# Kernel tuning notes

Hardware: AMD Instinct MI355X
Metric: run time of the kernel (lower is better)

Reference implementation:

```python
import math
import jax, jax.numpy as jnp
import numpy as np

HIDDEN = 768
HEADS = 12
HEAD_DIM = HIDDEN // HEADS  # 64
NUM_BUCKETS = 32            # T5-style relative position bias defaults
MAX_DIST = 128
EPS = 1e-6


def _rel_buckets(T):
    # T5 bidirectional relative-position bucketing, computed statically in numpy.
    ctx = np.arange(T)[:, None]
    mem = np.arange(T)[None, :]
    rp = mem - ctx                     # (T, T)
    nb = NUM_BUCKETS // 2
    ret = (rp > 0).astype(np.int64) * nb
    n = np.abs(rp)
    max_exact = nb // 2
    is_small = n < max_exact
    val_large = max_exact + (
        np.log(np.maximum(n, 1) / max_exact) / math.log(MAX_DIST / max_exact) * (nb - max_exact)
    ).astype(np.int64)
    val_large = np.minimum(val_large, nb - 1)
    ret = ret + np.where(is_small, n, val_large)
    return ret  # (T, T) int


def _layernorm(x, scale, bias):
    mu = jnp.mean(x, axis=-1, keepdims=True)
    var = jnp.mean((x - mu) ** 2, axis=-1, keepdims=True)
    return (x - mu) * jax.lax.rsqrt(var + EPS) * scale + bias


def _rms_groupnorm(x, weight):
    # x: (N, C, H, W, D); RMS over (channels-in-group, spatial), per-channel scale.
    N, C, H, W, D = x.shape
    xg = x.reshape(N, HEADS, C // HEADS, H, W, D)
    ms = jnp.mean(xg * xg, axis=(2, 3, 4, 5), keepdims=True)
    xg = xg * jax.lax.rsqrt(ms + EPS)
    return xg.reshape(N, C, H, W, D) * weight[None, :, None, None, None]


def _forward(x, norm1_weight, input_head_weight, input_head_bias,
             qnorm_scale, qnorm_bias, knorm_scale, knorm_bias,
             rel_bias_table, output_head_weight, output_head_bias):
    T, B, C, H, W, D = x.shape
    residual = x
    xn = _rms_groupnorm(x.reshape(T * B, C, H, W, D), norm1_weight)
    # 1x1 conv QKV as channels-last matmul
    w_in = input_head_weight[:, :, 0, 0, 0]                       # (3C, C)
    xt = jnp.transpose(xn, (0, 2, 3, 4, 1))                        # (TB, H, W, D, C)
    qkv = xt @ w_in.T + input_head_bias                            # (TB, H, W, D, 3C)
    # '(t b) (he c) h w d -> (b h w d) he t c'  with c = 3*head_dim
    qkv = qkv.reshape(T, B, H, W, D, HEADS, 3 * HEAD_DIM)
    qkv = jnp.transpose(qkv, (1, 2, 3, 4, 5, 0, 6))                # (B,H,W,D,He,T,3hd)
    qkv = qkv.reshape(B * H * W * D, HEADS, T, 3 * HEAD_DIM)
    q, k, v = jnp.split(qkv, 3, axis=-1)                           # each (N, He, T, hd)
    q = _layernorm(q, qnorm_scale, qnorm_bias)
    k = _layernorm(k, knorm_scale, knorm_bias)
    # relative position bias (bidirectional)
    buckets = jnp.asarray(_rel_buckets(T))                         # (T, T)
    bias = jnp.transpose(rel_bias_table[buckets], (2, 0, 1))[None]  # (1, He, T, T)
    scale = 1.0 / math.sqrt(HEAD_DIM)
    attn = jax.nn.softmax(jnp.einsum('bhsc,bhtc->bhst', q, k) * scale + bias, axis=-1)
    out = jnp.einsum('bhst,bhtc->bhsc', attn, v)                   # (N, He, T, hd)
    # '(b h w d) he t c -> (t b) (he c) h w d'
    out = out.reshape(B, H, W, D, HEADS, T, HEAD_DIM)
    out = jnp.transpose(out, (5, 0, 4, 6, 1, 2, 3))                # (T,B,He,hd,H,W,D)
    out = out.reshape(T * B, C, H, W, D)
    # output 1x1 conv
    w_out = output_head_weight[:, :, 0, 0, 0]                      # (C, C)
    ot = jnp.transpose(out, (0, 2, 3, 4, 1)) @ w_out.T + output_head_bias
    y = jnp.transpose(ot, (0, 4, 1, 2, 3)).reshape(T, B, C, H, W, D)
    return y + residual


def setup_inputs() -> dict:
    key = jax.random.key(0)
    ks = jax.random.split(key, 4)
    T, B, C, H, W, D = 16, 1, HIDDEN, 16, 16, 8
    x = jax.random.normal(ks[0], (T, B, C, H, W, D), dtype=jnp.float32)
    lecun = 1.0 / math.sqrt(HIDDEN)
    return {
        'x': x,
        'norm1_weight': jnp.ones((HIDDEN,), jnp.float32),
        'input_head_weight': jax.random.normal(ks[1], (3 * HIDDEN, HIDDEN, 1, 1, 1), jnp.float32) * lecun,
        'input_head_bias': jnp.zeros((3 * HIDDEN,), jnp.float32),
        'qnorm_scale': jnp.ones((HEAD_DIM,), jnp.float32),
        'qnorm_bias': jnp.zeros((HEAD_DIM,), jnp.float32),
        'knorm_scale': jnp.ones((HEAD_DIM,), jnp.float32),
        'knorm_bias': jnp.zeros((HEAD_DIM,), jnp.float32),
        'rel_bias_table': jax.random.normal(ks[2], (NUM_BUCKETS, HEADS), jnp.float32) * 0.02,
        'output_head_weight': jax.random.normal(ks[3], (HIDDEN, HIDDEN, 1, 1, 1), jnp.float32) * lecun,
        'output_head_bias': jnp.zeros((HIDDEN,), jnp.float32),
    }


def reference(x, norm1_weight, input_head_weight, input_head_bias,
              qnorm_scale, qnorm_bias, knorm_scale, knorm_bias,
              rel_bias_table, output_head_weight, output_head_bias):
    return _forward(x, norm1_weight, input_head_weight, input_head_bias,
                    qnorm_scale, qnorm_bias, knorm_scale, knorm_bias,
                    rel_bias_table, output_head_weight, output_head_bias)
```

## Files before the change

### kernel.cpp

```cpp
#include <hip/hip_runtime.h>
#include <stdint.h>

#define Tt 16
#define Cc 768
#define Ss 2048
#define N1 2304
#define NH 12
#define HD 64
#define EPSV 1e-6f

typedef unsigned short ushort_t;
typedef __attribute__((ext_vector_type(8))) short short8;
typedef __attribute__((ext_vector_type(4))) short short4v;
typedef __attribute__((ext_vector_type(4))) float f32x4;

static __device__ __forceinline__ float b2f(unsigned short u) {
  union { unsigned int i; float f; } c;
  c.i = ((unsigned int)u) << 16;
  return c.f;
}
static __device__ __forceinline__ unsigned short f2b(float f) {
  union { float f; unsigned int i; } c;
  c.f = f;
  return (unsigned short)((c.i + 0x7fffu + ((c.i >> 16) & 1u)) >> 16);
}

static __device__ __forceinline__ void load8(const void* p, size_t eoff,
                                             int isf32, float* o) {
  if (isf32) {
    const float* f = (const float*)p + eoff;
    f32x4 a = *(const f32x4*)f;
    f32x4 b = *(const f32x4*)(f + 4);
    o[0] = a[0]; o[1] = a[1]; o[2] = a[2]; o[3] = a[3];
    o[4] = b[0]; o[5] = b[1]; o[6] = b[2]; o[7] = b[3];
  } else {
    short8 d = *(const short8*)((const ushort_t*)p + eoff);
#pragma unroll
    for (int e = 0; e < 8; e++) o[e] = b2f((unsigned short)d[e]);
  }
}
static __device__ __forceinline__ float load1(const void* p, size_t eoff, int isf32) {
  return isf32 ? ((const float*)p)[eoff] : b2f(((const ushort_t*)p)[eoff]);
}

#define GLP(p) ((const __attribute__((address_space(1))) void*)(p))
#define LDSP(p) ((__attribute__((address_space(3))) void*)(p))

__global__ __launch_bounds__(256) void detect_k(const ushort_t* __restrict__ x,
                                               int* __restrict__ flag) {
  __shared__ int sbad;
  if (threadIdx.x == 0) sbad = 0;
  __syncthreads();
  int bad = 0;
  for (int i = threadIdx.x; i < 65536; i += 256) {
    const unsigned int e = (x[i] >> 7) & 0xFFu;
    if (e == 0xFFu) bad = 1;
  }
  if (bad) atomicOr(&sbad, 1);
  __syncthreads();
  if (threadIdx.x == 0) flag[0] = sbad;
}

__global__ __launch_bounds__(256) void cvt_big_k(const void* __restrict__ src,
                                                ushort_t* __restrict__ dst,
                                                int n8, const int* __restrict__ flag) {
  const int isf32 = *flag;
  const int i = blockIdx.x * 256 + threadIdx.x;
  if (i >= n8) return;
  float o[8];
  load8(src, (size_t)i * 8, isf32, o);
  short8 v;
#pragma unroll
  for (int e = 0; e < 8; e++) v[e] = (short)f2b(o[e]);
  *(short8*)(dst + (size_t)i * 8) = v;
}

__global__ __launch_bounds__(256) void cvt_small_k(
    const void* w1, const void* bin, const void* bo, const void* qs,
    const void* qb, const void* ks, const void* kb, const void* relb,
    ushort_t* __restrict__ dst, const int* __restrict__ flag) {
  const int isf32 = *flag;
  const void* srcs[8] = {w1, bin, bo, qs, qb, ks, kb, relb};
  const int sizes[8] = {768, 2304, 768, 64, 64, 64, 64, 384};
  int off = 0;
#pragma unroll
  for (int s = 0; s < 8; s++) {
    for (int i = threadIdx.x; i < sizes[s]; i += 256)
      dst[off + i] = isf32 ? f2b(((const float*)srcs[s])[i])
                           : ((const ushort_t*)srcs[s])[i];
    off += sizes[s];
  }
}

__global__ __launch_bounds__(256) void rms_stats_k(
    const void* __restrict__ x, const int* __restrict__ flag,
    float* __restrict__ invrms) {
  const int isf32 = *flag;
  const int t = blockIdx.x / NH;
  const int g = blockIdx.x % NH;
  const size_t base = ((size_t)(t * Cc + g * 64)) * Ss;
  float ss = 0.f;
  for (int v = threadIdx.x; v < 16384; v += 256) {
    const int ci = v >> 8;
    const int sj = (v & 255) << 3;
    float o[8];
    load8(x, base + (size_t)ci * Ss + sj, isf32, o);
#pragma unroll
    for (int e = 0; e < 8; e++) ss += o[e] * o[e];
  }
#pragma unroll
  for (int m = 1; m < 64; m <<= 1) ss += __shfl_xor(ss, m);
  __shared__ float red[4];
  if ((threadIdx.x & 63) == 0) red[threadIdx.x >> 6] = ss;
  __syncthreads();
  if (threadIdx.x == 0) {
    float tot = red[0] + red[1] + red[2] + red[3];
    invrms[blockIdx.x] = rsqrtf(tot * (1.f / 131072.f) + EPSV);
  }
}

__global__ __launch_bounds__(256) void norm_chunk_k(
    const void* __restrict__ x, const int* __restrict__ flag,
    const ushort_t* __restrict__ w1, const float* __restrict__ invrms,
    ushort_t* __restrict__ xnc, int s0c, int chl) {
  __shared__ __align__(16) ushort_t tile[64][64];
  const int isf32 = *flag;
  const int t = blockIdx.z;
  const int c0 = blockIdx.y * 64;
  const int sl0 = blockIdx.x * 64;
  const float ir = invrms[t * NH + (c0 >> 6)];
  const int tid = threadIdx.x;
  for (int v = tid; v < 512; v += 256) {
    const int ci = v >> 3;
    const int q = v & 7;
    float o[8];
    load8(x, ((size_t)(t * Cc + c0 + ci)) * Ss + s0c + sl0 + q * 8, isf32, o);
    const float sc = ir * b2f(w1[c0 + ci]);
    short8 w;
#pragma unroll
    for (int e = 0; e < 8; e++) w[e] = (short)f2b(o[e] * sc);
    *(short8*)&tile[ci][(q ^ (ci >> 3)) * 8] = w;
  }
  __syncthreads();
  for (int v = tid; v < 512; v += 256) {
    const int sj = v >> 3;
    const int cb = (v & 7) * 8;
    const int sw = (sj >> 3) ^ (v & 7);
    const int so = sj & 7;
    short8 o;
#pragma unroll
    for (int e = 0; e < 8; e++) o[e] = (short)tile[cb + e][sw * 8 + so];
    *(short8*)(xnc + ((size_t)(t * chl + sl0 + sj)) * Cc + c0 + cb) = o;
  }
}

__global__ __launch_bounds__(256, 2) void gemm_qkv_k(
    const ushort_t* __restrict__ A, const ushort_t* __restrict__ Bw,
    const ushort_t* __restrict__ bias, ushort_t* __restrict__ Cout) {
  __shared__ __align__(16) ushort_t As[128 * 32];
  __shared__ __align__(16) ushort_t Bs[128 * 32];
  const int tid = threadIdx.x;
  const int bm0 = blockIdx.x * 128;
  const int bn0 = blockIdx.y * 128;
  const int lane = tid & 63;
  const int wave = tid >> 6;
  const int wm = (wave >> 1) << 6;
  const int wn = (wave & 1) << 6;
  f32x4 acc[4][4];
#pragma unroll
  for (int i = 0; i < 4; i++)
#pragma unroll
    for (int j = 0; j < 4; j++) acc[i][j] = (f32x4){0.f, 0.f, 0.f, 0.f};
  const int srow = tid >> 2;
  const int scol = (tid & 3) << 3;
  const ushort_t* ag = A + (size_t)(bm0 + srow) * Cc + scol;
  const ushort_t* bg = Bw + (size_t)(bn0 + srow) * Cc + scol;
  ushort_t* la = As + tid * 8;
  ushort_t* lb = Bs + tid * 8;
  const int frow = lane & 15;
  const int koff = (lane >> 4) << 3;
  for (int kt = 0; kt < Cc; kt += 32) {
    __syncthreads();
    __builtin_amdgcn_global_load_lds(GLP(ag + kt), LDSP(la), 16, 0, 0);
    __builtin_amdgcn_global_load_lds(GLP(ag + kt + 64 * Cc), LDSP(la + 2048), 16, 0, 0);
    __builtin_amdgcn_global_load_lds(GLP(bg + kt), LDSP(lb), 16, 0, 0);
    __builtin_amdgcn_global_load_lds(GLP(bg + kt + 64 * Cc), LDSP(lb + 2048), 16, 0, 0);
    __syncthreads();
    short8 af[4], bf[4];
#pragma unroll
    for (int i = 0; i < 4; i++)
      af[i] = *(const short8*)(As + (wm + i * 16 + frow) * 32 + koff);
#pragma unroll
    for (int j = 0; j < 4; j++)
      bf[j] = *(const short8*)(Bs + (wn + j * 16 + frow) * 32 + koff);
#pragma unroll
    for (int i = 0; i < 4; i++)
#pragma unroll
      for (int j = 0; j < 4; j++)
        acc[i][j] = __builtin_amdgcn_mfma_f32_16x16x32_bf16(af[i], bf[j], acc[i][j], 0, 0, 0);
  }
  const int mq = (lane >> 4) << 2;
  const int nl = lane & 15;
#pragma unroll
  for (int j = 0; j < 4; j++) {
    const int col = bn0 + wn + j * 16 + nl;
    const float bc = b2f(bias[col]);
#pragma unroll
    for (int i = 0; i < 4; i++) {
#pragma unroll
      for (int r = 0; r < 4; r++) {
        const int row = bm0 + wm + i * 16 + mq + r;
        Cout[(size_t)row * N1 + col] = f2b(acc[i][j][r] + bc);
      }
    }
  }
}

static __device__ __forceinline__ void rdA_q(short8 af[4][2], const ushort_t* base,
                                             int arow, int half, const int ckk[2]) {
#pragma unroll
  for (int mi = 0; mi < 4; mi++)
#pragma unroll
    for (int kk = 0; kk < 2; kk++)
      af[mi][kk] = *(const short8*)&base[arow + half * 4096 + mi * 1024 + ckk[kk]];
}
static __device__ __forceinline__ void rdB_q(short8 bf[2][2], const ushort_t* base,
                                             int brow, int nib, const int ckk[2]) {
#pragma unroll
  for (int ni = 0; ni < 2; ni++)
#pragma unroll
    for (int kk = 0; kk < 2; kk++)
      bf[ni][kk] = *(const short8*)&base[brow + (nib + ni) * 1024 + ckk[kk]];
}
template <int MIB, int NIB>
static __device__ __forceinline__ void mm8_q(f32x4 (&acc)[8][4], const short8 af[4][2],
                                             const short8 bf[2][2]) {
#pragma unroll
  for (int mi = 0; mi < 4; mi++)
#pragma unroll
    for (int ni = 0; ni < 2; ni++)
#pragma unroll
      for (int kk = 0; kk < 2; kk++)
        acc[MIB + mi][NIB + ni] = __builtin_amdgcn_mfma_f32_16x16x32_bf16(
            af[mi][kk], bf[ni][kk], acc[MIB + mi][NIB + ni], 0, 0, 0);
}

__global__ __launch_bounds__(512, 2) void gemm_qkv256_k(
    const ushort_t* __restrict__ A, const ushort_t* __restrict__ Bw,
    const ushort_t* __restrict__ bias, ushort_t* __restrict__ Cout) {
  __shared__ __align__(16) ushort_t lds[2][2][16384];
  const int tid = threadIdx.x;
  const int lane = tid & 63;
  const int wave = tid >> 6;
  const int wr = wave >> 2;
  const int wc = wave & 3;
  const int wg = ((int)blockIdx.x & 7) * 144 + ((int)blockIdx.x >> 3);
  const int bm0 = (wg / 9) * 256;
  const int bn0 = (wg % 9) * 256;
  const int srow = tid >> 3;
  const int scol = ((tid & 7) ^ (srow & 7)) << 3;
  const ushort_t* ag = A + (size_t)(bm0 + srow) * Cc + scol;
  const ushort_t* bg = Bw + (size_t)(bn0 + srow) * Cc + scol;
#define QSTG(p, kt) { \
    __builtin_amdgcn_global_load_lds(GLP(ag + (kt)), LDSP(&lds[p][0][tid * 8]), 16, 0, 0); \
    __builtin_amdgcn_global_load_lds(GLP(ag + 64 * Cc + (kt)), LDSP(&lds[p][0][4096 + tid * 8]), 16, 0, 0); \
    __builtin_amdgcn_global_load_lds(GLP(ag + 128 * Cc + (kt)), LDSP(&lds[p][0][8192 + tid * 8]), 16, 0, 0); \
    __builtin_amdgcn_global_load_lds(GLP(ag + 192 * Cc + (kt)), LDSP(&lds[p][0][12288 + tid * 8]), 16, 0, 0); \
    __builtin_amdgcn_global_load_lds(GLP(bg + (kt)), LDSP(&lds[p][1][tid * 8]), 16, 0, 0); \
    __builtin_amdgcn_global_load_lds(GLP(bg + 64 * Cc + (kt)), LDSP(&lds[p][1][4096 + tid * 8]), 16, 0, 0); \
    __builtin_amdgcn_global_load_lds(GLP(bg + 128 * Cc + (kt)), LDSP(&lds[p][1][8192 + tid * 8]), 16, 0, 0); \
    __builtin_amdgcn_global_load_lds(GLP(bg + 192 * Cc + (kt)), LDSP(&lds[p][1][12288 + tid * 8]), 16, 0, 0); \
  }
  const int koffb = (lane >> 4) << 4;
  const int lsw = (lane & 7) << 4;
  const int ckk[2] = {(koffb ^ lsw) >> 1, ((64 + koffb) ^ lsw) >> 1};
  const int arow = (wr * 128 + (lane & 15)) * 64;
  const int brow = (wc * 64 + (lane & 15)) * 64;
  f32x4 acc[8][4];
#pragma unroll
  for (int i = 0; i < 8; i++)
#pragma unroll
    for (int j = 0; j < 4; j++) acc[i][j] = (f32x4){0.f, 0.f, 0.f, 0.f};
  QSTG(0, 0);
  __syncthreads();
  for (int i = 0; i < 12; i++) {
    const int p = i & 1;
    if (i < 11) QSTG(p ^ 1, (i + 1) * 64);
    __builtin_amdgcn_sched_barrier(0);
    const ushort_t* Ab = &lds[p][0][0];
    const ushort_t* Bb = &lds[p][1][0];
    short8 af[4][2], bf0[2][2], bf1[2][2];
    rdA_q(af, Ab, arow, 0, ckk);
    rdB_q(bf0, Bb, brow, 0, ckk);
    __builtin_amdgcn_s_setprio(1);
    mm8_q<0, 0>(acc, af, bf0);
    __builtin_amdgcn_s_setprio(0);
    __builtin_amdgcn_sched_barrier(0);
    rdB_q(bf1, Bb, brow, 2, ckk);
    __builtin_amdgcn_s_setprio(1);
    mm8_q<0, 2>(acc, af, bf1);
    __builtin_amdgcn_s_setprio(0);
    __builtin_amdgcn_sched_barrier(0);
    rdA_q(af, Ab, arow, 1, ckk);
    __builtin_amdgcn_s_setprio(1);
    mm8_q<4, 0>(acc, af, bf0);
    __builtin_amdgcn_s_setprio(0);
    __builtin_amdgcn_sched_barrier(0);
    __builtin_amdgcn_s_setprio(1);
    mm8_q<4, 2>(acc, af, bf1);
    __builtin_amdgcn_s_setprio(0);
    if (i < 11) __syncthreads();
  }
  const int mq = (lane >> 4) << 2;
  const int nl = lane & 15;
#pragma unroll
  for (int ni = 0; ni < 4; ni++) {
    const int col = bn0 + wc * 64 + ni * 16 + nl;
    const float bc = b2f(bias[col]);
#pragma unroll
    for (int mi = 0; mi < 8; mi++) {
#pragma unroll
      for (int r = 0; r < 4; r++) {
        const int row = bm0 + wr * 128 + mi * 16 + mq + r;
        Cout[(size_t)row * N1 + col] = f2b(acc[mi][ni][r] + bc);
      }
    }
  }
#undef QSTG
}

__global__ __launch_bounds__(256) void attention_k(
    const ushort_t* __restrict__ qkvc, const ushort_t* __restrict__ qs,
    const ushort_t* __restrict__ qb, const ushort_t* __restrict__ ks,
    const ushort_t* __restrict__ kb, const ushort_t* __restrict__ relb,
    ushort_t* __restrict__ aoc, int chl) {
  __shared__ __align__(16) float qf[4][16][68];
  __shared__ __align__(16) float kf[4][16][68];
  __shared__ __align__(16) float vf[4][16][68];
  __shared__ __align__(16) float attw[4][16][20];
  __shared__ __align__(16) float lnw[4][64];
  const int tid = threadIdx.x;
  const int wave = tid >> 6;
  const int lane = tid & 63;
  if (tid < 64) {
    lnw[0][tid] = b2f(qs[tid]);
    lnw[1][tid] = b2f(qb[tid]);
    lnw[2][tid] = b2f(ks[tid]);
    lnw[3][tid] = b2f(kb[tid]);
  }
  const int p = blockIdx.x * 4 + wave;
  const int sl = p / 12;
  const int h = p - sl * 12;
  const ushort_t* src = qkvc + (size_t)sl * N1 + h * 192;
  const size_t tstride = (size_t)chl * N1;
#pragma unroll
  for (int t = 0; t < 16; t++) {
    const ushort_t* r = src + (size_t)t * tstride;
    qf[wave][t][lane] = b2f(r[lane]);
    kf[wave][t][lane] = b2f(r[64 + lane]);
    vf[wave][t][lane] = b2f(r[128 + lane]);
  }
  __syncthreads();
  {
    const int row = lane >> 1;
    const int half = lane & 1;
    float* buf = (row < 16) ? &qf[wave][row][0] : &kf[wave][row - 16][0];
    const float* sc = (row < 16) ? lnw[0] : lnw[2];
    const float* bi = (row < 16) ? lnw[1] : lnw[3];
    f32x4* bp = (f32x4*)(buf + half * 32);
    f32x4 v4[8];
    float s = 0.f;
#pragma unroll
    for (int q4 = 0; q4 < 8; q4++) {
      v4[q4] = bp[q4];
      s += v4[q4][0] + v4[q4][1] + v4[q4][2] + v4[q4][3];
    }
    s += __shfl_xor(s, 1);
    const float mu = s * (1.f / 64.f);
    float va = 0.f;
#pragma unroll
    for (int q4 = 0; q4 < 8; q4++) {
#pragma unroll
      for (int e = 0; e < 4; e++) {
        const float d = v4[q4][e] - mu;
        va += d * d;
      }
    }
    va += __shfl_xor(va, 1);
    const float rs = rsqrtf(va * (1.f / 64.f) + EPSV);
    const f32x4* sc4 = (const f32x4*)(sc + half * 32);
    const f32x4* bi4 = (const f32x4*)(bi + half * 32);
#pragma unroll
    for (int q4 = 0; q4 < 8; q4++) {
      f32x4 scv = sc4[q4], biv = bi4[q4], o;
#pragma unroll
      for (int e = 0; e < 4; e++) o[e] = (v4[q4][e] - mu) * rs * scv[e] + biv[e];
      bp[q4] = o;
    }
  }
  __syncthreads();
  const int g = lane >> 4;
  const int t2 = lane & 15;
#pragma unroll
  for (int it = 0; it < 4; it++) {
    const int t1 = it * 4 + g;
    const f32x4* qrow = (const f32x4*)&qf[wave][t1][0];
    const f32x4* krow = (const f32x4*)&kf[wave][t2][0];
    float sco = 0.f;
#pragma unroll
    for (int q4 = 0; q4 < 16; q4++) {
      f32x4 a = qrow[q4], b = krow[q4];
      sco += a[0] * b[0] + a[1] * b[1] + a[2] * b[2] + a[3] * b[3];
    }
    const int rp = t2 - t1;
    int bkt = (rp > 0) ? 16 : 0;
    const int n = (rp < 0) ? -rp : rp;
    if (n < 8) {
      bkt += n;
    } else {
      int vl = 8 + (int)(__logf((float)n * 0.125f) * 2.8853900817779268f);
      bkt += (vl < 15) ? vl : 15;
    }
    sco = sco * 0.125f + b2f(relb[bkt * NH + h]);
    float mx = sco;
#pragma unroll
    for (int m = 8; m >= 1; m >>= 1) mx = fmaxf(mx, __shfl_xor(mx, m));
    const float ex = __expf(sco - mx);
    float sm = ex;
#pragma unroll
    for (int m = 8; m >= 1; m >>= 1) sm += __shfl_xor(sm, m);
    attw[wave][t1][t2] = ex / sm;
  }
  __syncthreads();
  const int jq = lane & 15;
#pragma unroll
  for (int it = 0; it < 4; it++) {
    const int t1 = it * 4 + g;
    const f32x4* arow2 = (const f32x4*)&attw[wave][t1][0];
    f32x4 o = (f32x4){0.f, 0.f, 0.f, 0.f};
#pragma unroll
    for (int tq = 0; tq < 4; tq++) {
      f32x4 aw = arow2[tq];
#pragma unroll
      for (int e = 0; e < 4; e++) {
        f32x4 vv = *(const f32x4*)&vf[wave][tq * 4 + e][jq * 4];
        o[0] += aw[e] * vv[0];
        o[1] += aw[e] * vv[1];
        o[2] += aw[e] * vv[2];
        o[3] += aw[e] * vv[3];
      }
    }
    short4v st;
#pragma unroll
    for (int e = 0; e < 4; e++) st[e] = (short)f2b(o[e]);
    *(short4v*)(aoc + ((size_t)(t1 * chl + sl)) * Cc + h * HD + jq * 4) = st;
  }
}

__global__ __launch_bounds__(256, 2) void gemm_out_k(
    const ushort_t* __restrict__ A, const ushort_t* __restrict__ Bm,
    const ushort_t* __restrict__ bias, const void* __restrict__ xres,
    const int* __restrict__ flag, float* __restrict__ y, int s0c,
    int chl, int lgchl) {
  __shared__ __align__(16) ushort_t As[128 * 32];
  __shared__ __align__(16) ushort_t Bs[128 * 32];
  const int isf32 = *flag;
  const int tid = threadIdx.x;
  int bmt = blockIdx.x, bnt = blockIdx.y;
  {
    const int nwg = gridDim.x * gridDim.y;
    if ((nwg & 7) == 0) {
      const int hw = (int)blockIdx.x + (int)blockIdx.y * gridDim.x;
      const int cpx = nwg >> 3;
      const int w = (hw & 7) * cpx + (hw >> 3);
      bmt = w % gridDim.x;
      bnt = w / gridDim.x;
    }
  }
  const int bm0 = bmt * 128;
  const int bn0 = bnt * 128;
  const int lane = tid & 63;
  const int wave = tid >> 6;
  const int wm = (wave >> 1) << 6;
  const int wn = (wave & 1) << 6;
  f32x4 acc[4][4];
#pragma unroll
  for (int i = 0; i < 4; i++)
#pragma unroll
    for (int j = 0; j < 4; j++) acc[i][j] = (f32x4){0.f, 0.f, 0.f, 0.f};
  const int srow = tid >> 2;
  const int scol = (tid & 3) << 3;
  const ushort_t* ag = A + (size_t)(bm0 + srow) * Cc + scol;
  const ushort_t* bg = Bm + (size_t)(bn0 + srow) * Cc + scol;
  ushort_t* la = As + tid * 8;
  ushort_t* lb = Bs + tid * 8;
  const int frow = lane & 15;
  const int koff = (lane >> 4) << 3;
  for (int kt = 0; kt < Cc; kt += 32) {
    __syncthreads();
    __builtin_amdgcn_global_load_lds(GLP(ag + kt), LDSP(la), 16, 0, 0);
    __builtin_amdgcn_global_load_lds(GLP(ag + kt + 64 * Cc), LDSP(la + 2048), 16, 0, 0);
    __builtin_amdgcn_global_load_lds(GLP(bg + kt), LDSP(lb), 16, 0, 0);
    __builtin_amdgcn_global_load_lds(GLP(bg + kt + 64 * Cc), LDSP(lb + 2048), 16, 0, 0);
    __syncthreads();
    short8 af[4], bf[4];
#pragma unroll
    for (int i = 0; i < 4; i++)
      af[i] = *(const short8*)(As + (wm + i * 16 + frow) * 32 + koff);
#pragma unroll
    for (int j = 0; j < 4; j++)
      bf[j] = *(const short8*)(Bs + (wn + j * 16 + frow) * 32 + koff);
#pragma unroll
    for (int i = 0; i < 4; i++)
#pragma unroll
      for (int j = 0; j < 4; j++)
        acc[i][j] = __builtin_amdgcn_mfma_f32_16x16x32_bf16(af[i], bf[j], acc[i][j], 0, 0, 0);
  }
  const int mq = (lane >> 4) << 2;
  const int nl = lane & 15;
#pragma unroll
  for (int j = 0; j < 4; j++) {
    const int col = bn0 + wn + j * 16 + nl;
    const int t = col >> lgchl;
    const int sp = s0c + (col & (chl - 1));
#pragma unroll
    for (int i = 0; i < 4; i++) {
#pragma unroll
      for (int r = 0; r < 4; r++) {
        const int cch = bm0 + wm + i * 16 + mq + r;
        const size_t off = ((size_t)(t * Cc + cch)) * Ss + sp;
        y[off] = acc[i][j][r] + b2f(bias[cch]) + load1(xres, off, isf32);
      }
    }
  }
}

extern "C" void kernel_launch(void* const* d_in, const int* in_sizes, int n_in,
                              void* d_out, int out_size, void* d_ws, size_t ws_size,
                              hipStream_t stream) {
  (void)in_sizes; (void)n_in; (void)out_size;
  const void* x   = d_in[0];
  const void* w1  = d_in[1];
  const void* win = d_in[2];
  const void* bin = d_in[3];
  const void* qsc = d_in[4];
  const void* qbi = d_in[5];
  const void* ksc = d_in[6];
  const void* kbi = d_in[7];
  const void* rbt = d_in[8];
  const void* wo  = d_in[9];
  const void* bo  = d_in[10];
  float* y = (float*)d_out;

  char* ws = (char*)d_ws;
  int* flag      = (int*)ws;
  ushort_t* smallw = (ushort_t*)(ws + 4096);
  ushort_t* w1b  = smallw;
  ushort_t* binb = smallw + 768;
  ushort_t* bob  = smallw + 3072;
  ushort_t* qsb  = smallw + 3840;
  ushort_t* qbb  = smallw + 3904;
  ushort_t* ksb  = smallw + 3968;
  ushort_t* kbb  = smallw + 4032;
  ushort_t* relbb = smallw + 4096;
  float* invrms  = (float*)(ws + 1024);
  ushort_t* winb = (ushort_t*)(ws + 20480);
  ushort_t* wob  = (ushort_t*)(ws + 3559424);
  const size_t fixed = 4739072;

  const size_t per_row = (size_t)(Cc * 2 + N1 * 2 + Cc * 2);
  int chl = Ss;
  while (chl > 64 && fixed + (size_t)Tt * chl * per_row > ws_size) chl >>= 1;
  int lgchl = 0;
  while ((1 << (lgchl + 1)) <= chl) lgchl++;

  ushort_t* xnc  = (ushort_t*)(ws + fixed);
  ushort_t* qkvc = xnc + (size_t)Tt * chl * Cc;
  ushort_t* aoc  = qkvc + (size_t)Tt * chl * N1;

  detect_k<<<1, 256, 0, stream>>>((const ushort_t*)x, flag);
  cvt_small_k<<<1, 256, 0, stream>>>(w1, bin, bo, qsc, qbi, ksc, kbi, rbt, smallw, flag);
  cvt_big_k<<<1769472 / 8 / 256, 256, 0, stream>>>(win, winb, 1769472 / 8, flag);
  cvt_big_k<<<589824 / 8 / 256, 256, 0, stream>>>(wo, wob, 589824 / 8, flag);
  rms_stats_k<<<dim3(Tt * NH), 256, 0, stream>>>(x, flag, invrms);
  for (int s0c = 0; s0c < Ss; s0c += chl) {
    norm_chunk_k<<<dim3(chl / 64, Cc / 64, Tt), 256, 0, stream>>>(x, flag, w1b, invrms, xnc, s0c, chl);
    if (chl == Ss) {
      gemm_qkv256_k<<<dim3(1152), 512, 0, stream>>>(xnc, winb, binb, qkvc);
    } else {
      gemm_qkv_k<<<dim3(Tt * chl / 128, N1 / 128), 256, 0, stream>>>(xnc, winb, binb, qkvc);
    }
    attention_k<<<dim3(chl * NH / 4), 256, 0, stream>>>(qkvc, qsb, qbb, ksb, kbb, relbb, aoc, chl);
    gemm_out_k<<<dim3(Cc / 128, Tt * chl / 128), 256, 0, stream>>>(wob, aoc, bob, x, flag, y, s0c, chl, lgchl);
  }
}
```

Baseline: 685.6 us.

## Restructure QKV GEMM into k-half staged phases with interleaved async loads

The 256x256 QKV GEMM is reorganised so each 64-wide k-tile is split into two 32-wide halves stored in separate LDS sub-buffers with a new XOR swizzle. Global-to-LDS loads for the next tile are issued in small chunks between MFMA phases, and partial vmcnt waits plus raw s_barrier replace the whole-tile __syncthreads. The goal is to overlap memory traffic with MFMA work more finely and cut stalls at the barrier. It adds many more barriers per iteration and depends on manual vmcnt counts being correct.

```diff
diff --git a/kernel.cpp b/kernel.cpp
--- a/kernel.cpp
+++ b/kernel.cpp
@@ -216,39 +216,35 @@
   }
 }
 
-static __device__ __forceinline__ void rdA_q(short8 af[4][2], const ushort_t* base,
-                                             int arow, int half, const int ckk[2]) {
+static __device__ __forceinline__ void rdA4(short8 af[4], const ushort_t* base,
+                                            int ar, int mib, int ck) {
 #pragma unroll
   for (int mi = 0; mi < 4; mi++)
-#pragma unroll
-    for (int kk = 0; kk < 2; kk++)
-      af[mi][kk] = *(const short8*)&base[arow + half * 4096 + mi * 1024 + ckk[kk]];
-}
-static __device__ __forceinline__ void rdB_q(short8 bf[2][2], const ushort_t* base,
-                                             int brow, int nib, const int ckk[2]) {
-#pragma unroll
-  for (int ni = 0; ni < 2; ni++)
-#pragma unroll
-    for (int kk = 0; kk < 2; kk++)
-      bf[ni][kk] = *(const short8*)&base[brow + (nib + ni) * 1024 + ckk[kk]];
-}
-template <int MIB, int NIB>
-static __device__ __forceinline__ void mm8_q(f32x4 (&acc)[8][4], const short8 af[4][2],
-                                             const short8 bf[2][2]) {
+    af[mi] = *(const short8*)&base[(ar + (mib + mi) * 16) * 32 + ck];
+}
+static __device__ __forceinline__ void rdB4(short8 bf[4], const ushort_t* base,
+                                            int br, int ck) {
+#pragma unroll
+  for (int ni = 0; ni < 4; ni++)
+    bf[ni] = *(const short8*)&base[(br + ni * 16) * 32 + ck];
+}
+template <int MIB>
+static __device__ __forceinline__ void mmq(f32x4 (&acc)[8][4], const short8 af[4],
+                                           const short8 bf[4]) {
 #pragma unroll
   for (int mi = 0; mi < 4; mi++)
 #pragma unroll
-    for (int ni = 0; ni < 2; ni++)
-#pragma unroll
-      for (int kk = 0; kk < 2; kk++)
-        acc[MIB + mi][NIB + ni] = __builtin_amdgcn_mfma_f32_16x16x32_bf16(
-            af[mi][kk], bf[ni][kk], acc[MIB + mi][NIB + ni], 0, 0, 0);
-}
+    for (int ni = 0; ni < 4; ni++)
+      acc[MIB + mi][ni] = __builtin_amdgcn_mfma_f32_16x16x32_bf16(
+          af[mi], bf[ni], acc[MIB + mi][ni], 0, 0, 0);
+}
+#define QPH_BAR { __builtin_amdgcn_sched_barrier(0); __builtin_amdgcn_s_barrier(); \
+                  __builtin_amdgcn_sched_barrier(0); }
 
 __global__ __launch_bounds__(512, 2) void gemm_qkv256_k(
     const ushort_t* __restrict__ A, const ushort_t* __restrict__ Bw,
     const ushort_t* __restrict__ bias, ushort_t* __restrict__ Cout) {
-  __shared__ __align__(16) ushort_t lds[2][2][16384];
+  __shared__ __align__(16) ushort_t lds[2][2][2][8192];
   const int tid = threadIdx.x;
   const int lane = tid & 63;
   const int wave = tid >> 6;
@@ -257,59 +253,100 @@
   const int wg = ((int)blockIdx.x & 7) * 144 + ((int)blockIdx.x >> 3);
   const int bm0 = (wg / 9) * 256;
   const int bn0 = (wg % 9) * 256;
-  const int srow = tid >> 3;
-  const int scol = ((tid & 7) ^ (srow & 7)) << 3;
+  const int srow = tid >> 2;
+  const int scol = ((tid & 3) ^ ((tid >> 3) & 3)) << 3;
   const ushort_t* ag = A + (size_t)(bm0 + srow) * Cc + scol;
   const ushort_t* bg = Bw + (size_t)(bn0 + srow) * Cc + scol;
-#define QSTG(p, kt) { \
-    __builtin_amdgcn_global_load_lds(GLP(ag + (kt)), LDSP(&lds[p][0][tid * 8]), 16, 0, 0); \
-    __builtin_amdgcn_global_load_lds(GLP(ag + 64 * Cc + (kt)), LDSP(&lds[p][0][4096 + tid * 8]), 16, 0, 0); \
-    __builtin_amdgcn_global_load_lds(GLP(ag + 128 * Cc + (kt)), LDSP(&lds[p][0][8192 + tid * 8]), 16, 0, 0); \
-    __builtin_amdgcn_global_load_lds(GLP(ag + 192 * Cc + (kt)), LDSP(&lds[p][0][12288 + tid * 8]), 16, 0, 0); \
-    __builtin_amdgcn_global_load_lds(GLP(bg + (kt)), LDSP(&lds[p][1][tid * 8]), 16, 0, 0); \
-    __builtin_amdgcn_global_load_lds(GLP(bg + 64 * Cc + (kt)), LDSP(&lds[p][1][4096 + tid * 8]), 16, 0, 0); \
-    __builtin_amdgcn_global_load_lds(GLP(bg + 128 * Cc + (kt)), LDSP(&lds[p][1][8192 + tid * 8]), 16, 0, 0); \
-    __builtin_amdgcn_global_load_lds(GLP(bg + 192 * Cc + (kt)), LDSP(&lds[p][1][12288 + tid * 8]), 16, 0, 0); \
-  }
-  const int koffb = (lane >> 4) << 4;
-  const int lsw = (lane & 7) << 4;
-  const int ckk[2] = {(koffb ^ lsw) >> 1, ((64 + koffb) ^ lsw) >> 1};
-  const int arow = (wr * 128 + (lane & 15)) * 64;
-  const int brow = (wc * 64 + (lane & 15)) * 64;
+#define STGA(p, kh, kt) { \
+    __builtin_amdgcn_global_load_lds(GLP(ag + (kt) + (kh) * 32), \
+        LDSP(&lds[p][0][kh][tid * 8]), 16, 0, 0); \
+    __builtin_amdgcn_global_load_lds(GLP(ag + 128 * Cc + (kt) + (kh) * 32), \
+        LDSP(&lds[p][0][kh][4096 + tid * 8]), 16, 0, 0); \
+  }
+#define STGB(p, kh, kt) { \
+    __builtin_amdgcn_global_load_lds(GLP(bg + (kt) + (kh) * 32), \
+        LDSP(&lds[p][1][kh][tid * 8]), 16, 0, 0); \
+    __builtin_amdgcn_global_load_lds(GLP(bg + 128 * Cc + (kt) + (kh) * 32), \
+        LDSP(&lds[p][1][kh][4096 + tid * 8]), 16, 0, 0); \
+  }
+  const int ck = (((lane >> 4) ^ ((lane >> 1) & 3)) << 3);
+  const int ar = wr * 128 + (lane & 15);
+  const int br = wc * 64 + (lane & 15);
   f32x4 acc[8][4];
 #pragma unroll
   for (int i = 0; i < 8; i++)
 #pragma unroll
     for (int j = 0; j < 4; j++) acc[i][j] = (f32x4){0.f, 0.f, 0.f, 0.f};
-  QSTG(0, 0);
-  __syncthreads();
-  for (int i = 0; i < 12; i++) {
-    const int p = i & 1;
-    if (i < 11) QSTG(p ^ 1, (i + 1) * 64);
+  short8 af[4], bf[4];
+  STGA(0, 0, 0); STGB(0, 0, 0); STGA(0, 1, 0); STGB(0, 1, 0);
+  asm volatile("s_waitcnt vmcnt(4)");
+  QPH_BAR;
+  for (int t = 0; t < 11; t++) {
+    const int p = t & 1;
+    const int q = p ^ 1;
+    const int kt = (t + 1) * 64;
+    rdA4(af, &lds[p][0][0][0], ar, 0, ck);
+    rdB4(bf, &lds[p][1][0][0], br, ck);
+    STGA(q, 0, kt);
+    QPH_BAR;
+    __builtin_amdgcn_s_setprio(1);
+    mmq<0>(acc, af, bf);
+    __builtin_amdgcn_s_setprio(0);
+    QPH_BAR;
+    rdA4(af, &lds[p][0][0][0], ar, 4, ck);
+    STGB(q, 0, kt);
+    QPH_BAR;
+    __builtin_amdgcn_s_setprio(1);
+    mmq<4>(acc, af, bf);
+    __builtin_amdgcn_s_setprio(0);
     __builtin_amdgcn_sched_barrier(0);
-    const ushort_t* Ab = &lds[p][0][0];
-    const ushort_t* Bb = &lds[p][1][0];
-    short8 af[4][2], bf0[2][2], bf1[2][2];
-    rdA_q(af, Ab, arow, 0, ckk);
-    rdB_q(bf0, Bb, brow, 0, ckk);
-    __builtin_amdgcn_s_setprio(1);
-    mm8_q<0, 0>(acc, af, bf0);
+    asm volatile("s_waitcnt vmcnt(4)");
+    QPH_BAR;
+    rdA4(af, &lds[p][0][1][0], ar, 0, ck);
+    rdB4(bf, &lds[p][1][1][0], br, ck);
+    STGA(q, 1, kt);
+    QPH_BAR;
+    __builtin_amdgcn_s_setprio(1);
+    mmq<0>(acc, af, bf);
+    __builtin_amdgcn_s_setprio(0);
+    QPH_BAR;
+    rdA4(af, &lds[p][0][1][0], ar, 4, ck);
+    STGB(q, 1, kt);
+    QPH_BAR;
+    __builtin_amdgcn_s_setprio(1);
+    mmq<4>(acc, af, bf);
     __builtin_amdgcn_s_setprio(0);
     __builtin_amdgcn_sched_barrier(0);
-    rdB_q(bf1, Bb, brow, 2, ckk);
-    __builtin_amdgcn_s_setprio(1);
-    mm8_q<0, 2>(acc, af, bf1);
+    asm volatile("s_waitcnt vmcnt(4)");
+    QPH_BAR;
+  }
+  {
+    rdA4(af, &lds[1][0][0][0], ar, 0, ck);
+    rdB4(bf, &lds[1][1][0][0], br, ck);
+    QPH_BAR;
+    __builtin_amdgcn_s_setprio(1);
+    mmq<0>(acc, af, bf);
+    __builtin_amdgcn_s_setprio(0);
+    QPH_BAR;
+    rdA4(af, &lds[1][0][0][0], ar, 4, ck);
+    QPH_BAR;
+    __builtin_amdgcn_s_setprio(1);
+    mmq<4>(acc, af, bf);
     __builtin_amdgcn_s_setprio(0);
     __builtin_amdgcn_sched_barrier(0);
-    rdA_q(af, Ab, arow, 1, ckk);
-    __builtin_amdgcn_s_setprio(1);
-    mm8_q<4, 0>(acc, af, bf0);
-    __builtin_amdgcn_s_setprio(0);
-    __builtin_amdgcn_sched_barrier(0);
-    __builtin_amdgcn_s_setprio(1);
-    mm8_q<4, 2>(acc, af, bf1);
-    __builtin_amdgcn_s_setprio(0);
-    if (i < 11) __syncthreads();
+    asm volatile("s_waitcnt vmcnt(0)");
+    QPH_BAR;
+    rdA4(af, &lds[1][0][1][0], ar, 0, ck);
+    rdB4(bf, &lds[1][1][1][0], br, ck);
+    QPH_BAR;
+    __builtin_amdgcn_s_setprio(1);
+    mmq<0>(acc, af, bf);
+    __builtin_amdgcn_s_setprio(0);
+    QPH_BAR;
+    rdA4(af, &lds[1][0][1][0], ar, 4, ck);
+    __builtin_amdgcn_s_setprio(1);
+    mmq<4>(acc, af, bf);
+    __builtin_amdgcn_s_setprio(0);
   }
   const int mq = (lane >> 4) << 2;
   const int nl = lane & 15;
@@ -326,7 +363,8 @@
       }
     }
   }
-#undef QSTG
+#undef STGA
+#undef STGB
 }
 
 __global__ __launch_bounds__(256) void attention_k(
```

Result: no change. 691.6 us (+0.9%).
